# Kernel optimization log

Measured on AMD Instinct MI355X. Metric: run time of the kernel, lower is better.

## Reference

```python
import jax, jax.numpy as jnp
import numpy as np

NB, T, NS, NC = 512, 128, 32, 16
NSC = NS + NC


def setup_inputs() -> dict:
    key = jax.random.key(0)
    k1, k2, k3, k4, k5, k6 = jax.random.split(key, 6)
    # Q must be PSD per-step (as in the pypose example: Q = Q.mT @ Q), plus a
    # small ridge so Quu is well-conditioned for pinv.
    Qr = jax.random.normal(k1, (NB, T, NSC, NSC), jnp.float32)
    Q = jnp.einsum('btji,btjk->btik', Qr, Qr) / NSC + 0.1 * jnp.eye(NSC, dtype=jnp.float32)
    p = jax.random.normal(k2, (NB, T, NSC), jnp.float32)
    # Mildly stable LTI dynamics so the T=128 rollout stays bounded.
    A0 = 0.5 * jnp.eye(NS, dtype=jnp.float32) + 0.1 * jax.random.normal(k3, (NS, NS), jnp.float32) / np.sqrt(NS)
    A = jnp.broadcast_to(A0, (NB, NS, NS)).astype(jnp.float32)
    Bm = jax.random.normal(k4, (NB, NS, NC), jnp.float32) / np.sqrt(NS)
    c1 = jax.random.normal(k5, (NB, NS), jnp.float32)
    x_init = jax.random.normal(k6, (NB, NS), jnp.float32)
    return {"x_init": x_init, "Q": Q, "p": p, "A": A, "Bm": Bm, "c1": c1}


def _bmv(M, v):
    return jnp.einsum('bij,bj->bi', M, v)


def reference(x_init, Q, p, A, Bm, c1):
    # F = [A B] : [NB, NS, NSC] (time-invariant LTI system)
    F = jnp.concatenate([A, Bm], axis=-1)
    FT = jnp.swapaxes(F, -1, -2)

    Qtm = jnp.moveaxis(Q, 1, 0)  # [T, NB, NSC, NSC]
    ptm = jnp.moveaxis(p, 1, 0)  # [T, NB, NSC]

    # ---- backward Riccati recursion (t = T-1 .. 0) ----
    def bwd_step(carry, inp):
        V, v = carry  # V: [NB,NS,NS], v: [NB,NS]; zero at t = T-1
        Qt_in, pt = inp
        Qt = Qt_in + FT @ V @ F
        qt = pt + _bmv(FT, v) + _bmv(FT, _bmv(V, c1))
        Qxx, Qxu = Qt[..., :NS, :NS], Qt[..., :NS, NS:]
        Qux, Quu = Qt[..., NS:, :NS], Qt[..., NS:, NS:]
        qx, qu = qt[..., :NS], qt[..., NS:]
        Quu_inv = jnp.linalg.pinv(Quu)
        Kt = -(Quu_inv @ Qux)                 # [NB, NC, NS]
        kt = -_bmv(Quu_inv, qu)               # [NB, NC]
        KtT = jnp.swapaxes(Kt, -1, -2)
        V_new = Qxx + Qxu @ Kt + KtT @ Qux + KtT @ Quu @ Kt
        v_new = qx + _bmv(Qxu, kt) + _bmv(KtT, qu) + _bmv(KtT @ Quu, kt)
        return (V_new, v_new), (Kt, kt)

    V0 = jnp.zeros((NB, NS, NS), Q.dtype)
    v0 = jnp.zeros((NB, NS), Q.dtype)
    _, (Ks, ks) = jax.lax.scan(bwd_step, (V0, v0), (Qtm, ptm), reverse=True)

    # ---- forward rollout (t = 0 .. T-1) ----
    def fwd_step(x, inp):
        Kt, kt, Qt, pt = inp
        ut = _bmv(Kt, x) + kt
        xu = jnp.concatenate([x, ut], axis=-1)
        x_next = _bmv(A, x) + _bmv(Bm, ut) + c1
        c = 0.5 * jnp.einsum('bi,bij,bj->b', xu, Qt, xu) + jnp.sum(xu * pt, axis=-1)
        return x_next, (x, ut, c)

    _, (xs, us, cs) = jax.lax.scan(fwd_step, x_init, (Ks, ks, Qtm, ptm))
    x = jnp.moveaxis(xs, 0, 1)   # [NB, T, NS], states x_0..x_{T-1}
    u = jnp.moveaxis(us, 0, 1)   # [NB, T, NC]
    cost = jnp.sum(cs, axis=0)   # [NB]
    return x, u, cost
```

## Files before the change

### kernel.cpp

```cpp
#include <hip/hip_runtime.h>

#define NB 512
#define T 128
#define NS 32
#define NC 16
#define NSC 48
#define PF 52
#define PV 36
#define PK 36

__device__ __forceinline__ float4 ld4(const float* p) { return *(const float4*)p; }
__device__ __forceinline__ void st4(float* p, float4 v) { *(float4*)p = v; }
__device__ __forceinline__ void fma4(float4& a, float s, float4 f) {
    a.x = fmaf(s, f.x, a.x); a.y = fmaf(s, f.y, a.y);
    a.z = fmaf(s, f.z, a.z); a.w = fmaf(s, f.w, a.w);
}
__device__ __forceinline__ float dot4(float4 a, float4 b) {
    return fmaf(a.x, b.x, fmaf(a.y, b.y, fmaf(a.z, b.z, a.w * b.w)));
}
__device__ __forceinline__ float rlane(float v, int l) {
    return __uint_as_float(__builtin_amdgcn_readlane(__float_as_uint(v), l));
}

__global__ __launch_bounds__(256, 2)
void lqr_backward(const float* __restrict__ Q,
                  const float* __restrict__ p,
                  const float* __restrict__ A,
                  const float* __restrict__ Bm,
                  const float* __restrict__ c1,
                  float* __restrict__ Kws,
                  float* __restrict__ kws)
{
    const int b = blockIdx.x;
    const int tid = threadIdx.x;
    const int lane = tid & 63;
    const int wv = tid >> 6;

    __shared__ __align__(16) float sF[NS][PF];
    __shared__ __align__(16) float sW[NS][PF];
    __shared__ __align__(16) float sQt[NSC][PF];
    __shared__ __align__(16) float sV[NS][PV];
    __shared__ __align__(16) float sKt[NC][PK];
    __shared__ __align__(16) float sz[NS];
    __shared__ __align__(16) float sqt[NSC];
    __shared__ __align__(16) float sv[NS];
    __shared__ __align__(16) float sc1[NS];
    __shared__ __align__(16) float skt[NC];

    for (int e = tid; e < NS * NSC; e += 256) {
        int i = e / NSC, j = e % NSC;
        sF[i][j] = (j < NS) ? A[(size_t)b * NS * NS + i * NS + j]
                            : Bm[(size_t)b * NS * NC + i * NC + (j - NS)];
    }
    for (int e = tid; e < NS * NS; e += 256) sV[e >> 5][e & 31] = 0.f;
    if (tid < NS) { sv[tid] = 0.f; sc1[tid] = c1[(size_t)b * NS + tid]; }
    __syncthreads();

    for (int t = T - 1; t >= 0; --t) {
        const float* Qg = Q + ((size_t)b * T + t) * NSC * NSC;

        float4 qgb0 = {0,0,0,0}, qgb1 = {0,0,0,0};
        float preg = 0.f;
        if (tid >= 160) {
            int ct = tid - 160;
            int i0b = NS + (ct / 12) * 2, j0b = (ct % 12) * 4;
            qgb0 = ld4(Qg + i0b * NSC + j0b);
            qgb1 = ld4(Qg + (i0b + 1) * NSC + j0b);
        }
        if (tid >= 64 && tid < 112) preg = p[((size_t)b * T + t) * NSC + (tid - 64)];
        if (tid < 192) {
            const int i0 = (tid / 12) * 2, j0 = (tid % 12) * 4;
            float4 a0 = {0,0,0,0}, a1 = {0,0,0,0};
            #pragma unroll 8
            for (int k = 0; k < NS; ++k) {
                float2 v2 = *(const float2*)&sV[k][i0];
                float4 f4 = ld4(&sF[k][j0]);
                fma4(a0, v2.x, f4); fma4(a1, v2.y, f4);
            }
            st4(&sW[i0][j0], a0); st4(&sW[i0 + 1][j0], a1);
        } else if (tid < 224) {
            int i = tid - 192;
            float a = sv[i];
            #pragma unroll
            for (int k0 = 0; k0 < NS; k0 += 4)
                a += dot4(ld4(&sV[i][k0]), ld4(&sc1[k0]));
            sz[i] = a;
        }
        __syncthreads();

        float4 qgc0 = {0,0,0,0}, qgc1 = {0,0,0,0};
        int i0c = 0, j0c = 0;
        if (tid >= 64 && tid < 192) {
            int ct = tid - 64; i0c = (ct / 8) * 2; j0c = (ct % 8) * 4;
            qgc0 = ld4(Qg + i0c * NSC + j0c);
            qgc1 = ld4(Qg + (i0c + 1) * NSC + j0c);
        }
        if (tid >= 160) {
            const int ct = tid - 160;
            const int i0b = NS + (ct / 12) * 2, j0b = (ct % 12) * 4;
            float4 a0 = qgb0, a1 = qgb1;
            #pragma unroll 8
            for (int k = 0; k < NS; ++k) {
                float2 f2 = *(const float2*)&sF[k][i0b];
                float4 w4 = ld4(&sW[k][j0b]);
                fma4(a0, f2.x, w4); fma4(a1, f2.y, w4);
            }
            st4(&sQt[i0b][j0b], a0); st4(&sQt[i0b + 1][j0b], a1);
        } else if (tid >= 64 && tid < 112) {
            int j = tid - 64;
            float a = preg;
            #pragma unroll 8
            for (int k = 0; k < NS; ++k) a = fmaf(sF[k][j], sz[k], a);
            sqt[j] = a;
        }
        __syncthreads();

        if (wv == 0) {
            float R[NC];
            if (lane < NC) {
                #pragma unroll
                for (int i = 0; i < NC; ++i) R[i] = sQt[NS + i][NS + lane];
            } else if (lane < NSC) {
                #pragma unroll
                for (int i = 0; i < NC; ++i) R[i] = sQt[NS + i][lane - NC];
            } else if (lane == NSC) {
                #pragma unroll
                for (int i = 0; i < NC; ++i) R[i] = sqt[NS + i];
            } else {
                #pragma unroll
                for (int i = 0; i < NC; ++i) R[i] = 0.f;
            }
            #pragma unroll
            for (int k = 0; k < NC; ++k) {
                float pk = rlane(R[k], k);
                float inv = __builtin_amdgcn_rcpf(pk);
                inv = inv * fmaf(-pk, inv, 2.0f);
                float tm = R[k] * inv;
                #pragma unroll
                for (int i = 0; i < NC; ++i) {
                    if (i == k) continue;
                    float cki = rlane(R[i], k);
                    R[i] = fmaf(-tm, cki, R[i]);
                }
                R[k] = tm;
            }
            if (lane >= NC && lane < NSC) {
                const int c = lane - NC;
                #pragma unroll
                for (int i = 0; i < NC; ++i) sKt[i][c] = -R[i];
            } else if (lane == NSC) {
                #pragma unroll
                for (int i = 0; i < NC; ++i) skt[i] = -R[i];
            }
        } else if (tid < 192) {
            float4 a0 = qgc0, a1 = qgc1;
            #pragma unroll 8
            for (int k = 0; k < NS; ++k) {
                float2 f2 = *(const float2*)&sF[k][i0c];
                float4 w4 = ld4(&sW[k][j0c]);
                fma4(a0, f2.x, w4); fma4(a1, f2.y, w4);
            }
            st4(&sQt[i0c][j0c], a0); st4(&sQt[i0c + 1][j0c], a1);
        }
        __syncthreads();

        if (tid < 128) {
            const int i0 = (tid / 8) * 2, j0 = (tid % 8) * 4;
            float4 a0 = ld4(&sQt[i0][j0]), a1 = ld4(&sQt[i0 + 1][j0]);
            #pragma unroll
            for (int k = 0; k < NC; ++k) {
                float2 q2 = *(const float2*)&sQt[NS + k][i0];
                float4 k4 = ld4(&sKt[k][j0]);
                fma4(a0, q2.x, k4); fma4(a1, q2.y, k4);
            }
            st4(&sV[i0][j0], a0); st4(&sV[i0 + 1][j0], a1);
        } else if (tid < 160) {
            float4* Kg4 = (float4*)(Kws + ((size_t)b * T + t) * NC * NS);
            int e = (tid - 128) * 4;
            #pragma unroll
            for (int q = 0; q < 4; ++q)
                Kg4[e + q] = ld4(&sKt[(e + q) >> 3][((e + q) & 7) * 4]);
        } else if (tid >= 192 && tid < 224) {
            int j = tid - 192;
            float a = sqt[j];
            #pragma unroll
            for (int k = 0; k < NC; ++k) a = fmaf(sQt[NS + k][j], skt[k], a);
            sv[j] = a;
        } else if (tid >= 224 && tid < 240) {
            kws[((size_t)b * T + t) * NC + (tid - 224)] = skt[tid - 224];
        }
        __syncthreads();
    }
}

__global__ __launch_bounds__(256, 2)
void lqr_forward(const float* __restrict__ x_init,
                 const float* __restrict__ Q,
                 const float* __restrict__ p,
                 const float* __restrict__ A,
                 const float* __restrict__ Bm,
                 const float* __restrict__ c1,
                 const float* __restrict__ Kws,
                 const float* __restrict__ kws,
                 float* __restrict__ out_x,
                 float* __restrict__ out_u,
                 float* __restrict__ out_cost)
{
    const int b = blockIdx.x;
    const int tid = threadIdx.x;
    const int lane = tid & 63;
    const int wv = tid >> 6;

    __shared__ __align__(16) float sK[2][8 * 576];
    __shared__ __align__(16) float sk[2][128];
    __shared__ __align__(16) float sxu[2][8][48];
    __shared__ float sred[4];

    float costAcc = 0.f;
    float4 Freg[12];
    float c1reg = 0.f, xu = 0.f;

    if (wv == 0) {
        const int i = lane & 31;
        const float* Ar = A + (size_t)b * NS * NS + i * NS;
        const float* Br = Bm + (size_t)b * NS * NC + i * NC;
        #pragma unroll
        for (int g = 0; g < 8; ++g) Freg[g] = ld4(Ar + g * 4);
        #pragma unroll
        for (int g = 0; g < 4; ++g) Freg[8 + g] = ld4(Br + g * 4);
        c1reg = c1[(size_t)b * NS + i];
        xu = x_init[(size_t)b * NS + i];
    } else {
        const float4* src = (const float4*)(Kws + (size_t)b * T * NC * NS);
        int ct = tid - 64;
        for (int idx = ct; idx < 1024; idx += 192) {
            int s = idx >> 7, rem = idx & 127, row = rem >> 3, jg = rem & 7;
            st4(&sK[0][s * 576 + row * 36 + jg * 4], src[idx]);
        }
        if (ct < 32) st4(&sk[0][ct * 4], ((const float4*)(kws + (size_t)b * T * NC))[ct]);
    }
    __syncthreads();

    for (int it = 0; it <= 16; ++it) {
        if (wv == 0) {
            if (it < 16) {
                const int buf = it & 1;
                for (int s = 0; s < 8; ++s) {
                    const float* kb = &sK[buf][s * 576 + (lane & 15) * 36];
                    float4 Kq[8];
                    #pragma unroll
                    for (int g = 0; g < 8; ++g) Kq[g] = ld4(kb + g * 4);
                    float ktv = sk[buf][s * 16 + (lane & 15)];

                    float u0 = 0.f, u1 = 0.f;
                    #pragma unroll
                    for (int g = 0; g < 8; ++g) {
                        float x0 = rlane(xu, 4 * g + 0);
                        float x1 = rlane(xu, 4 * g + 1);
                        float x2 = rlane(xu, 4 * g + 2);
                        float x3 = rlane(xu, 4 * g + 3);
                        u0 = fmaf(Kq[g].x, x0, u0); u1 = fmaf(Kq[g].y, x1, u1);
                        u0 = fmaf(Kq[g].z, x2, u0); u1 = fmaf(Kq[g].w, x3, u1);
                    }
                    if (lane >= NS && lane < NSC) xu = u0 + u1 + ktv;
                    if (lane < NSC) sxu[buf][s][lane] = xu;

                    float a0 = 0.f, a1 = 0.f;
                    #pragma unroll
                    for (int g = 0; g < 12; ++g) {
                        float x0 = rlane(xu, 4 * g + 0);
                        float x1 = rlane(xu, 4 * g + 1);
                        float x2 = rlane(xu, 4 * g + 2);
                        float x3 = rlane(xu, 4 * g + 3);
                        a0 = fmaf(Freg[g].x, x0, a0); a1 = fmaf(Freg[g].y, x1, a1);
                        a0 = fmaf(Freg[g].z, x2, a0); a1 = fmaf(Freg[g].w, x3, a1);
                    }
                    if (lane < NS) xu = a0 + a1 + c1reg;
                }
            }
        } else {
            const int ct = tid - 64;
            if (it < 15) {
                const int nbuf = (it + 1) & 1;
                const float4* src = (const float4*)(Kws + ((size_t)b * T + (it + 1) * 8) * NC * NS);
                for (int idx = ct; idx < 1024; idx += 192) {
                    int s = idx >> 7, rem = idx & 127, row = rem >> 3, jg = rem & 7;
                    st4(&sK[nbuf][s * 576 + row * 36 + jg * 4], src[idx]);
                }
                if (ct < 32) st4(&sk[nbuf][ct * 4],
                                 ((const float4*)(kws + ((size_t)b * T + (it + 1) * 8) * NC))[ct]);
            }
            if (it >= 1) {
                const int buf = (it - 1) & 1;
                const int c = it - 1;
                for (int s = 0; s < 8; ++s) {
                    const int t = c * 8 + s;
                    const float* Qg = Q + ((size_t)b * T + t) * NSC * NSC;
                    #pragma unroll
                    for (int rr0 = 0; rr0 < 3; ++rr0) {
                        int rr = ct * 3 + rr0;
                        float4 q = ld4(Qg + rr * 4);
                        int i = rr / 12, j0 = (rr % 12) * 4;
                        float4 xv = ld4(&sxu[buf][s][j0]);
                        costAcc = fmaf(0.5f * sxu[buf][s][i], dot4(q, xv), costAcc);
                    }
                    if (ct < NSC) {
                        float xuv = sxu[buf][s][ct];
                        costAcc = fmaf(p[((size_t)b * T + t) * NSC + ct], xuv, costAcc);
                        if (ct < NS) out_x[((size_t)b * T + t) * NS + ct] = xuv;
                        else         out_u[((size_t)b * T + t) * NC + (ct - NS)] = xuv;
                    }
                }
            }
        }
        __syncthreads();
    }

    for (int off = 32; off > 0; off >>= 1)
        costAcc += __shfl_down(costAcc, off, 64);
    if ((tid & 63) == 0) sred[wv] = costAcc;
    __syncthreads();
    if (tid == 0) out_cost[b] = (sred[0] + sred[1]) + (sred[2] + sred[3]);
}

extern "C" void kernel_launch(void* const* d_in, const int* in_sizes, int n_in,
                              void* d_out, int out_size, void* d_ws, size_t ws_size,
                              hipStream_t stream) {
    const float* x_init = (const float*)d_in[0];
    const float* Q      = (const float*)d_in[1];
    const float* p      = (const float*)d_in[2];
    const float* A      = (const float*)d_in[3];
    const float* Bm     = (const float*)d_in[4];
    const float* c1     = (const float*)d_in[5];

    float* out      = (float*)d_out;
    float* out_x    = out;
    float* out_u    = out + (size_t)NB * T * NS;
    float* out_cost = out + (size_t)NB * T * (NS + NC);

    float* Kws = (float*)d_ws;
    float* kws = Kws + (size_t)NB * T * NC * NS;

    lqr_backward<<<NB, 256, 0, stream>>>(Q, p, A, Bm, c1, Kws, kws);
    lqr_forward<<<NB, 256, 0, stream>>>(x_init, Q, p, A, Bm, c1, Kws, kws,
                                        out_x, out_u, out_cost);
}
```

Baseline: 1.584 ms.

## Prefetch next-step Q in backward pass and split forward into chain and cost kernels

```diff
diff --git a/kernel.cpp b/kernel.cpp
--- a/kernel.cpp
+++ b/kernel.cpp
@@ -54,20 +54,33 @@
     }
     for (int e = tid; e < NS * NS; e += 256) sV[e >> 5][e & 31] = 0.f;
     if (tid < NS) { sv[tid] = 0.f; sc1[tid] = c1[(size_t)b * NS + tid]; }
+
+    const int i0b = NS + (tid / 12) * 2, j0b = (tid % 12) * 4;
+    const int ctx = tid - 96;
+    const int i0x = (ctx >> 3) * 2, j0x = (ctx & 7) * 4;
+    const int ctq = tid - 224;
+
+    float4 pf0 = {0,0,0,0}, pf1 = {0,0,0,0};
+    float pp0 = 0.f, pp1 = 0.f;
+
+    #define PREFETCH(tt) do {                                                   \
+        const float* Qn = Q + ((size_t)b * T + (tt)) * NSC * NSC;               \
+        if (tid < 96) {                                                         \
+            pf0 = ld4(Qn + i0b * NSC + j0b);                                    \
+            pf1 = ld4(Qn + (i0b + 1) * NSC + j0b);                              \
+        } else if (tid < 224) {                                                 \
+            pf0 = ld4(Qn + i0x * NSC + j0x);                                    \
+            pf1 = ld4(Qn + (i0x + 1) * NSC + j0x);                              \
+        } else {                                                                \
+            pp0 = p[((size_t)b * T + (tt)) * NSC + ctq];                        \
+            if (ctq < 16) pp1 = p[((size_t)b * T + (tt)) * NSC + 32 + ctq];     \
+        }                                                                       \
+    } while (0)
+
+    PREFETCH(T - 1);
     __syncthreads();
 
     for (int t = T - 1; t >= 0; --t) {
-        const float* Qg = Q + ((size_t)b * T + t) * NSC * NSC;
-
-        float4 qgb0 = {0,0,0,0}, qgb1 = {0,0,0,0};
-        float preg = 0.f;
-        if (tid >= 160) {
-            int ct = tid - 160;
-            int i0b = NS + (ct / 12) * 2, j0b = (ct % 12) * 4;
-            qgb0 = ld4(Qg + i0b * NSC + j0b);
-            qgb1 = ld4(Qg + (i0b + 1) * NSC + j0b);
-        }
-        if (tid >= 64 && tid < 112) preg = p[((size_t)b * T + t) * NSC + (tid - 64)];
         if (tid < 192) {
             const int i0 = (tid / 12) * 2, j0 = (tid % 12) * 4;
             float4 a0 = {0,0,0,0}, a1 = {0,0,0,0};
@@ -88,17 +101,8 @@
         }
         __syncthreads();
 
-        float4 qgc0 = {0,0,0,0}, qgc1 = {0,0,0,0};
-        int i0c = 0, j0c = 0;
-        if (tid >= 64 && tid < 192) {
-            int ct = tid - 64; i0c = (ct / 8) * 2; j0c = (ct % 8) * 4;
-            qgc0 = ld4(Qg + i0c * NSC + j0c);
-            qgc1 = ld4(Qg + (i0c + 1) * NSC + j0c);
-        }
-        if (tid >= 160) {
-            const int ct = tid - 160;
-            const int i0b = NS + (ct / 12) * 2, j0b = (ct % 12) * 4;
-            float4 a0 = qgb0, a1 = qgb1;
+        if (tid < 96) {
+            float4 a0 = pf0, a1 = pf1;
             #pragma unroll 8
             for (int k = 0; k < NS; ++k) {
                 float2 f2 = *(const float2*)&sF[k][i0b];
@@ -106,12 +110,26 @@
                 fma4(a0, f2.x, w4); fma4(a1, f2.y, w4);
             }
             st4(&sQt[i0b][j0b], a0); st4(&sQt[i0b + 1][j0b], a1);
-        } else if (tid >= 64 && tid < 112) {
-            int j = tid - 64;
-            float a = preg;
+        } else if (tid < 224) {
+            float4 a0 = pf0, a1 = pf1;
             #pragma unroll 8
-            for (int k = 0; k < NS; ++k) a = fmaf(sF[k][j], sz[k], a);
-            sqt[j] = a;
+            for (int k = 0; k < NS; ++k) {
+                float2 f2 = *(const float2*)&sF[k][i0x];
+                float4 w4 = ld4(&sW[k][j0x]);
+                fma4(a0, f2.x, w4); fma4(a1, f2.y, w4);
+            }
+            st4(&sQt[i0x][j0x], a0); st4(&sQt[i0x + 1][j0x], a1);
+        } else {
+            float a = pp0;
+            #pragma unroll 8
+            for (int k = 0; k < NS; ++k) a = fmaf(sF[k][ctq], sz[k], a);
+            sqt[ctq] = a;
+            if (ctq < 16) {
+                float a2 = pp1;
+                #pragma unroll 8
+                for (int k = 0; k < NS; ++k) a2 = fmaf(sF[k][32 + ctq], sz[k], a2);
+                sqt[32 + ctq] = a2;
+            }
         }
         __syncthreads();
 
@@ -152,175 +170,194 @@
                 #pragma unroll
                 for (int i = 0; i < NC; ++i) skt[i] = -R[i];
             }
-        } else if (tid < 192) {
-            float4 a0 = qgc0, a1 = qgc1;
-            #pragma unroll 8
-            for (int k = 0; k < NS; ++k) {
-                float2 f2 = *(const float2*)&sF[k][i0c];
-                float4 w4 = ld4(&sW[k][j0c]);
-                fma4(a0, f2.x, w4); fma4(a1, f2.y, w4);
-            }
-            st4(&sQt[i0c][j0c], a0); st4(&sQt[i0c + 1][j0c], a1);
-        }
-        __syncthreads();
-
-        if (tid < 128) {
-            const int i0 = (tid / 8) * 2, j0 = (tid % 8) * 4;
-            float4 a0 = ld4(&sQt[i0][j0]), a1 = ld4(&sQt[i0 + 1][j0]);
-            #pragma unroll
-            for (int k = 0; k < NC; ++k) {
-                float2 q2 = *(const float2*)&sQt[NS + k][i0];
-                float4 k4 = ld4(&sKt[k][j0]);
-                fma4(a0, q2.x, k4); fma4(a1, q2.y, k4);
-            }
-            st4(&sV[i0][j0], a0); st4(&sV[i0 + 1][j0], a1);
-        } else if (tid < 160) {
+        } else if (t > 0) {
+            PREFETCH(t - 1);
+        }
+        __syncthreads();
+
+        if (tid < 64) {
+            if (t > 0) PREFETCH(t - 1);
+        } else if (tid < 96) {
             float4* Kg4 = (float4*)(Kws + ((size_t)b * T + t) * NC * NS);
-            int e = (tid - 128) * 4;
+            int e = (tid - 64) * 4;
             #pragma unroll
             for (int q = 0; q < 4; ++q)
                 Kg4[e + q] = ld4(&sKt[(e + q) >> 3][((e + q) & 7) * 4]);
-        } else if (tid >= 192 && tid < 224) {
-            int j = tid - 192;
-            float a = sqt[j];
-            #pragma unroll
-            for (int k = 0; k < NC; ++k) a = fmaf(sQt[NS + k][j], skt[k], a);
-            sv[j] = a;
-        } else if (tid >= 224 && tid < 240) {
-            kws[((size_t)b * T + t) * NC + (tid - 224)] = skt[tid - 224];
-        }
-        __syncthreads();
-    }
-}
-
-__global__ __launch_bounds__(256, 2)
-void lqr_forward(const float* __restrict__ x_init,
-                 const float* __restrict__ Q,
-                 const float* __restrict__ p,
-                 const float* __restrict__ A,
-                 const float* __restrict__ Bm,
-                 const float* __restrict__ c1,
-                 const float* __restrict__ Kws,
-                 const float* __restrict__ kws,
-                 float* __restrict__ out_x,
-                 float* __restrict__ out_u,
-                 float* __restrict__ out_cost)
+            if (tid < 68)
+                ((float4*)(kws + ((size_t)b * T + t) * NC))[tid - 64] =
+                    ld4(&skt[(tid - 64) * 4]);
+        } else if (tid < 224) {
+            float4 a0 = ld4(&sQt[i0x][j0x]), a1 = ld4(&sQt[i0x + 1][j0x]);
+            #pragma unroll
+            for (int k = 0; k < NC; ++k) {
+                float2 q2 = *(const float2*)&sQt[NS + k][i0x];
+                float4 k4 = ld4(&sKt[k][j0x]);
+                fma4(a0, q2.x, k4); fma4(a1, q2.y, k4);
+            }
+            st4(&sV[i0x][j0x], a0); st4(&sV[i0x + 1][j0x], a1);
+        } else {
+            float a = sqt[ctq];
+            #pragma unroll
+            for (int k = 0; k < NC; ++k) a = fmaf(sQt[NS + k][ctq], skt[k], a);
+            sv[ctq] = a;
+        }
+        __syncthreads();
+    }
+    #undef PREFETCH
+}
+
+__global__ __launch_bounds__(64)
+void lqr_chain(const float* __restrict__ x_init,
+               const float* __restrict__ A,
+               const float* __restrict__ Bm,
+               const float* __restrict__ c1,
+               const float* __restrict__ Kws,
+               const float* __restrict__ kws,
+               float* __restrict__ out_x,
+               float* __restrict__ out_u,
+               float* __restrict__ out_cost)
 {
     const int b = blockIdx.x;
-    const int tid = threadIdx.x;
-    const int lane = tid & 63;
-    const int wv = tid >> 6;
-
-    __shared__ __align__(16) float sK[2][8 * 576];
-    __shared__ __align__(16) float sk[2][128];
-    __shared__ __align__(16) float sxu[2][8][48];
-    __shared__ float sred[4];
-
-    float costAcc = 0.f;
+    const int lane = threadIdx.x;
+
+    __shared__ __align__(16) float sxu[2][64];
+
+    if (lane == 0) out_cost[b] = 0.f;
+
     float4 Freg[12];
-    float c1reg = 0.f, xu = 0.f;
-
-    if (wv == 0) {
-        const int i = lane & 31;
-        const float* Ar = A + (size_t)b * NS * NS + i * NS;
-        const float* Br = Bm + (size_t)b * NS * NC + i * NC;
+    float c1reg = 0.f, xv = 0.f;
+    if (lane < 32) {
+        const float* Ar = A + (size_t)b * NS * NS + lane * NS;
+        const float* Br = Bm + (size_t)b * NS * NC + lane * NC;
         #pragma unroll
         for (int g = 0; g < 8; ++g) Freg[g] = ld4(Ar + g * 4);
         #pragma unroll
         for (int g = 0; g < 4; ++g) Freg[8 + g] = ld4(Br + g * 4);
-        c1reg = c1[(size_t)b * NS + i];
-        xu = x_init[(size_t)b * NS + i];
-    } else {
-        const float4* src = (const float4*)(Kws + (size_t)b * T * NC * NS);
-        int ct = tid - 64;
-        for (int idx = ct; idx < 1024; idx += 192) {
-            int s = idx >> 7, rem = idx & 127, row = rem >> 3, jg = rem & 7;
-            st4(&sK[0][s * 576 + row * 36 + jg * 4], src[idx]);
-        }
-        if (ct < 32) st4(&sk[0][ct * 4], ((const float4*)(kws + (size_t)b * T * NC))[ct]);
+        c1reg = c1[(size_t)b * NS + lane];
+        xv = x_init[(size_t)b * NS + lane];
+        sxu[0][lane] = xv;
+    }
+
+    const int r = lane - 48;
+    const float* Kbase = Kws + (size_t)b * T * NC * NS;
+    const float* kbase = kws + (size_t)b * T * NC;
+    float4 KA[8], KB[8];
+    float kA = 0.f, kB = 0.f;
+    if (lane >= 48) {
+        #pragma unroll
+        for (int g = 0; g < 8; ++g) KA[g] = ld4(Kbase + r * NS + g * 4);
+        kA = kbase[r];
+        #pragma unroll
+        for (int g = 0; g < 8; ++g) KB[g] = ld4(Kbase + NC * NS + r * NS + g * 4);
+        kB = kbase[NC + r];
     }
     __syncthreads();
 
-    for (int it = 0; it <= 16; ++it) {
-        if (wv == 0) {
-            if (it < 16) {
-                const int buf = it & 1;
-                for (int s = 0; s < 8; ++s) {
-                    const float* kb = &sK[buf][s * 576 + (lane & 15) * 36];
-                    float4 Kq[8];
-                    #pragma unroll
-                    for (int g = 0; g < 8; ++g) Kq[g] = ld4(kb + g * 4);
-                    float ktv = sk[buf][s * 16 + (lane & 15)];
-
-                    float u0 = 0.f, u1 = 0.f;
-                    #pragma unroll
-                    for (int g = 0; g < 8; ++g) {
-                        float x0 = rlane(xu, 4 * g + 0);
-                        float x1 = rlane(xu, 4 * g + 1);
-                        float x2 = rlane(xu, 4 * g + 2);
-                        float x3 = rlane(xu, 4 * g + 3);
-                        u0 = fmaf(Kq[g].x, x0, u0); u1 = fmaf(Kq[g].y, x1, u1);
-                        u0 = fmaf(Kq[g].z, x2, u0); u1 = fmaf(Kq[g].w, x3, u1);
-                    }
-                    if (lane >= NS && lane < NSC) xu = u0 + u1 + ktv;
-                    if (lane < NSC) sxu[buf][s][lane] = xu;
-
-                    float a0 = 0.f, a1 = 0.f;
-                    #pragma unroll
-                    for (int g = 0; g < 12; ++g) {
-                        float x0 = rlane(xu, 4 * g + 0);
-                        float x1 = rlane(xu, 4 * g + 1);
-                        float x2 = rlane(xu, 4 * g + 2);
-                        float x3 = rlane(xu, 4 * g + 3);
-                        a0 = fmaf(Freg[g].x, x0, a0); a1 = fmaf(Freg[g].y, x1, a1);
-                        a0 = fmaf(Freg[g].z, x2, a0); a1 = fmaf(Freg[g].w, x3, a1);
-                    }
-                    if (lane < NS) xu = a0 + a1 + c1reg;
-                }
-            }
-        } else {
-            const int ct = tid - 64;
-            if (it < 15) {
-                const int nbuf = (it + 1) & 1;
-                const float4* src = (const float4*)(Kws + ((size_t)b * T + (it + 1) * 8) * NC * NS);
-                for (int idx = ct; idx < 1024; idx += 192) {
-                    int s = idx >> 7, rem = idx & 127, row = rem >> 3, jg = rem & 7;
-                    st4(&sK[nbuf][s * 576 + row * 36 + jg * 4], src[idx]);
-                }
-                if (ct < 32) st4(&sk[nbuf][ct * 4],
-                                 ((const float4*)(kws + ((size_t)b * T + (it + 1) * 8) * NC))[ct]);
-            }
-            if (it >= 1) {
-                const int buf = (it - 1) & 1;
-                const int c = it - 1;
-                for (int s = 0; s < 8; ++s) {
-                    const int t = c * 8 + s;
-                    const float* Qg = Q + ((size_t)b * T + t) * NSC * NSC;
-                    #pragma unroll
-                    for (int rr0 = 0; rr0 < 3; ++rr0) {
-                        int rr = ct * 3 + rr0;
-                        float4 q = ld4(Qg + rr * 4);
-                        int i = rr / 12, j0 = (rr % 12) * 4;
-                        float4 xv = ld4(&sxu[buf][s][j0]);
-                        costAcc = fmaf(0.5f * sxu[buf][s][i], dot4(q, xv), costAcc);
-                    }
-                    if (ct < NSC) {
-                        float xuv = sxu[buf][s][ct];
-                        costAcc = fmaf(p[((size_t)b * T + t) * NSC + ct], xuv, costAcc);
-                        if (ct < NS) out_x[((size_t)b * T + t) * NS + ct] = xuv;
-                        else         out_u[((size_t)b * T + t) * NC + (ct - NS)] = xuv;
-                    }
-                }
-            }
-        }
-        __syncthreads();
+    for (int t = 0; t < T; t += 2) {
+        if (lane >= 48) {
+            float u0 = kA, u1 = 0.f;
+            #pragma unroll
+            for (int g = 0; g < 8; g += 2) {
+                u0 += dot4(KA[g],     ld4(&sxu[0][g * 4]));
+                u1 += dot4(KA[g + 1], ld4(&sxu[0][g * 4 + 4]));
+            }
+            float u = u0 + u1;
+            sxu[0][NS + r] = u;
+            out_u[((size_t)b * T + t) * NC + r] = u;
+            const int tl = (t + 2 < T) ? t + 2 : T - 1;
+            const float* Kr = Kbase + (size_t)tl * NC * NS + r * NS;
+            #pragma unroll
+            for (int g = 0; g < 8; ++g) KA[g] = ld4(Kr + g * 4);
+            kA = kbase[(size_t)tl * NC + r];
+        }
+        __syncthreads();
+        if (lane < 32) {
+            out_x[((size_t)b * T + t) * NS + lane] = xv;
+            float a0 = c1reg, a1 = 0.f;
+            #pragma unroll
+            for (int g = 0; g < 12; g += 2) {
+                a0 += dot4(Freg[g],     ld4(&sxu[0][g * 4]));
+                a1 += dot4(Freg[g + 1], ld4(&sxu[0][g * 4 + 4]));
+            }
+            xv = a0 + a1;
+            sxu[1][lane] = xv;
+        }
+        __syncthreads();
+
+        if (lane >= 48) {
+            float u0 = kB, u1 = 0.f;
+            #pragma unroll
+            for (int g = 0; g < 8; g += 2) {
+                u0 += dot4(KB[g],     ld4(&sxu[1][g * 4]));
+                u1 += dot4(KB[g + 1], ld4(&sxu[1][g * 4 + 4]));
+            }
+            float u = u0 + u1;
+            sxu[1][NS + r] = u;
+            out_u[((size_t)b * T + t + 1) * NC + r] = u;
+            const int tl = (t + 3 < T) ? t + 3 : T - 1;
+            const float* Kr = Kbase + (size_t)tl * NC * NS + r * NS;
+            #pragma unroll
+            for (int g = 0; g < 8; ++g) KB[g] = ld4(Kr + g * 4);
+            kB = kbase[(size_t)tl * NC + r];
+        }
+        __syncthreads();
+        if (lane < 32) {
+            out_x[((size_t)b * T + t + 1) * NS + lane] = xv;
+            float a0 = c1reg, a1 = 0.f;
+            #pragma unroll
+            for (int g = 0; g < 12; g += 2) {
+                a0 += dot4(Freg[g],     ld4(&sxu[1][g * 4]));
+                a1 += dot4(Freg[g + 1], ld4(&sxu[1][g * 4 + 4]));
+            }
+            xv = a0 + a1;
+            sxu[0][lane] = xv;
+        }
+        __syncthreads();
+    }
+}
+
+#define CT 64
+__global__ __launch_bounds__(256, 4)
+void lqr_cost(const float* __restrict__ Q,
+              const float* __restrict__ p,
+              const float* __restrict__ out_x,
+              const float* __restrict__ out_u,
+              float* __restrict__ out_cost)
+{
+    const int blk = blockIdx.x;
+    const int b = blk >> 1;
+    const int t0 = (blk & 1) * CT;
+    const int tid = threadIdx.x;
+
+    __shared__ __align__(16) float sxu[CT][NSC];
+    __shared__ float sred[4];
+
+    const float4* gx = (const float4*)(out_x + ((size_t)b * T + t0) * NS);
+    const float4* gu = (const float4*)(out_u + ((size_t)b * T + t0) * NC);
+    for (int q = tid; q < CT * 8; q += 256) st4(&sxu[q >> 3][(q & 7) * 4], gx[q]);
+    for (int q = tid; q < CT * 4; q += 256) st4(&sxu[q >> 2][NS + (q & 3) * 4], gu[q]);
+    __syncthreads();
+
+    float acc = 0.f;
+    const float4* Qf4 = (const float4*)(Q + ((size_t)b * T + t0) * NSC * NSC);
+    for (int q = tid; q < CT * 576; q += 256) {
+        int t = q / 576, rem = q - t * 576;
+        int i = rem / 12, jg = rem - i * 12;
+        float4 qv = Qf4[q];
+        acc = fmaf(0.5f * sxu[t][i], dot4(qv, ld4(&sxu[t][jg * 4])), acc);
+    }
+    const float* pg = p + ((size_t)b * T + t0) * NSC;
+    for (int e = tid; e < CT * NSC; e += 256) {
+        int t = e / NSC, j = e - t * NSC;
+        acc = fmaf(pg[e], sxu[t][j], acc);
     }
 
     for (int off = 32; off > 0; off >>= 1)
-        costAcc += __shfl_down(costAcc, off, 64);
-    if ((tid & 63) == 0) sred[wv] = costAcc;
+        acc += __shfl_down(acc, off, 64);
+    if ((tid & 63) == 0) sred[tid >> 6] = acc;
     __syncthreads();
-    if (tid == 0) out_cost[b] = (sred[0] + sred[1]) + (sred[2] + sred[3]);
+    if (tid == 0)
+        atomicAdd(out_cost + b, (sred[0] + sred[1]) + (sred[2] + sred[3]));
 }
 
 extern "C" void kernel_launch(void* const* d_in, const int* in_sizes, int n_in,
@@ -342,6 +379,7 @@
     float* kws = Kws + (size_t)NB * T * NC * NS;
 
     lqr_backward<<<NB, 256, 0, stream>>>(Q, p, A, Bm, c1, Kws, kws);
-    lqr_forward<<<NB, 256, 0, stream>>>(x_init, Q, p, A, Bm, c1, Kws, kws,
-                                        out_x, out_u, out_cost);
-}
+    lqr_chain<<<NB, 64, 0, stream>>>(x_init, A, Bm, c1, Kws, kws,
+                                     out_x, out_u, out_cost);
+    lqr_cost<<<NB * 2, 256, 0, stream>>>(Q, p, out_x, out_u, out_cost);
+}
```

After: 1.552 ms. -2.0%, faster.
